# Optimization experiments

Hardware: AMD Instinct MI355X
Metric: run time of the kernel (lower is better)

Reference implementation:

```python
import jax, jax.numpy as jnp
import numpy as np

B, T, C = 4, 2048, 1024
H = 16
D = C // H  # head_dim = 64


def setup_inputs() -> dict:
    key = jax.random.key(0)
    ks = jax.random.split(key, 9)
    s = 1.0 / np.sqrt(C)
    return {
        "x": jax.random.normal(ks[0], (B, T, C), dtype=jnp.float32),
        "Wq": jax.random.normal(ks[1], (C, C), dtype=jnp.float32) * s,
        "bq": jnp.zeros((C,), dtype=jnp.float32),
        "Wk": jax.random.normal(ks[2], (C, C), dtype=jnp.float32) * s,
        "bk": jnp.zeros((C,), dtype=jnp.float32),
        "Wv": jax.random.normal(ks[3], (C, C), dtype=jnp.float32) * s,
        "bv": jnp.zeros((C,), dtype=jnp.float32),
        "Wp": jax.random.normal(ks[4], (C, C), dtype=jnp.float32) * s,
        "bp": jnp.zeros((C,), dtype=jnp.float32),
    }


def reference(x, Wq, bq, Wk, bk, Wv, bv, Wp, bp):
    # Linear projections; reshape to [B, H, T, D]
    def split_heads(y):
        return y.reshape(B, T, H, D).transpose(0, 2, 1, 3)

    q = split_heads(x @ Wq + bq)
    k = split_heads(x @ Wk + bk)
    v = split_heads(x @ Wv + bv)

    scale = 1.0 / np.sqrt(D)
    att = jnp.einsum('bhqd,bhkd->bhqk', q, k) * scale  # [B,H,T,T]
    att = jax.nn.softmax(att, axis=-1)
    # dropout with p=0.0 is identity
    out = jnp.einsum('bhqk,bhkd->bhqd', att, v)        # [B,H,T,D]
    out = out.transpose(0, 2, 1, 3).reshape(B, T, C)
    return out @ Wp + bp
```

## Files before the change

### kernel.cpp

```cpp
#include <hip/hip_runtime.h>


#define B_ 4
#define T_ 2048
#define C_ 1024
#define H_ 16
#define D_ 64

#define QSCALE 0.18033688011112042f

typedef float  f32x4  __attribute__((ext_vector_type(4)));
typedef __bf16 bf16x8 __attribute__((ext_vector_type(8)));
typedef __bf16 bf16x4 __attribute__((ext_vector_type(4)));
typedef __bf16 bf16x2 __attribute__((ext_vector_type(2)));
typedef unsigned uint2v __attribute__((ext_vector_type(2)));

typedef const __attribute__((address_space(1))) void gv_t;
typedef __attribute__((address_space(3))) void lds_t;

__device__ __forceinline__ void async_load16(const void* g, void* l) {
  __builtin_amdgcn_global_load_lds((gv_t*)g, (lds_t*)l, 16, 0, 0);
}

__device__ __forceinline__ float fast_exp2(float x) {
#if __has_builtin(__builtin_amdgcn_exp2f)
  return __builtin_amdgcn_exp2f(x);
#else
  return exp2f(x);
#endif
}

__device__ __forceinline__ void pl16_swap(unsigned& a, unsigned& b) {
#if __has_builtin(__builtin_amdgcn_permlane16_swap)
  uint2v r = __builtin_amdgcn_permlane16_swap(a, b, false, false);
  a = r[0];
  b = r[1];
#else
  asm("v_permlane16_swap_b32 %0, %1" : "+v"(a), "+v"(b));
#endif
}

__global__ __launch_bounds__(256) void cast_f32_bf16(
    const float* __restrict__ in, __bf16* __restrict__ out, int n) {
  int i = (blockIdx.x * 256 + threadIdx.x) * 8;
  if (i >= n) return;
  float4 a = *(const float4*)(in + i);
  float4 b = *(const float4*)(in + i + 4);
  bf16x8 o;
  o[0] = (__bf16)a.x; o[1] = (__bf16)a.y; o[2] = (__bf16)a.z; o[3] = (__bf16)a.w;
  o[4] = (__bf16)b.x; o[5] = (__bf16)b.y; o[6] = (__bf16)b.z; o[7] = (__bf16)b.w;
  *(bf16x8*)(out + i) = o;
}

__global__ __launch_bounds__(256) void transpose_cast_w(
    const float* __restrict__ W0, const float* __restrict__ W1,
    const float* __restrict__ W2, const float* __restrict__ W3,
    __bf16* __restrict__ out) {
  int z = blockIdx.z;
  const float* W = (z == 0) ? W0 : (z == 1) ? W1 : (z == 2) ? W2 : W3;
  __bf16* o = out + (size_t)z * (C_ * C_);
  __shared__ __align__(16) __bf16 sT[64][72];
  int tid = threadIdx.x;
  int n0 = blockIdx.x * 64, k0 = blockIdx.y * 64;
#pragma unroll
  for (int i = 0; i < 4; i++) {
    int s = tid + i * 256;
    int kr = s >> 4, nc = (s & 15) * 4;
    float4 v = *(const float4*)&W[(size_t)(k0 + kr) * C_ + n0 + nc];
    bf16x4 t;
    t[0] = (__bf16)v.x; t[1] = (__bf16)v.y; t[2] = (__bf16)v.z; t[3] = (__bf16)v.w;
    *(bf16x4*)&sT[kr][nc] = t;
  }
  __syncthreads();
#pragma unroll
  for (int i = 0; i < 2; i++) {
    int s = tid + i * 256;
    int nr = s >> 3, kc = (s & 7) * 8;
    bf16x8 ov;
#pragma unroll
    for (int j = 0; j < 8; j++) ov[j] = sT[kc + j][nr];
    *(bf16x8*)&o[(size_t)(n0 + nr) * C_ + k0 + kc] = ov;
  }
}

template <typename OutT, int EPI>
__device__ __forceinline__ void gemm_body(
    const __bf16* __restrict__ A, const __bf16* __restrict__ Bt,
    const float* __restrict__ bias, OutT* __restrict__ C, int M, int N, int K,
    float scale) {
  __shared__ __align__(16) __bf16 sA[128 * 32];
  __shared__ __align__(16) __bf16 sB[128 * 32];
  int tid = threadIdx.x, lane = tid & 63, wave = tid >> 6;
  int lr = lane & 15, quad = lane >> 4;
  int m0 = blockIdx.y * 128, n0 = blockIdx.x * 128;
  int wm = (wave & 1) * 64, wn = (wave >> 1) * 64;

  const f32x4 zero = {0.f, 0.f, 0.f, 0.f};
  f32x4 acc[4][4];
#pragma unroll
  for (int i = 0; i < 4; i++)
#pragma unroll
    for (int j = 0; j < 4; j++) acc[i][j] = zero;

  for (int k0 = 0; k0 < K; k0 += 32) {
    __syncthreads();
#pragma unroll
    for (int i = 0; i < 2; i++) {
      int s = tid + i * 256;
      int r = s >> 2, c8 = (s & 3) * 8;
      async_load16(A + (size_t)(m0 + r) * K + k0 + c8, &sA[s * 8]);
      async_load16(Bt + (size_t)(n0 + r) * K + k0 + c8, &sB[s * 8]);
    }
    __syncthreads();
    bf16x8 af[4], bfr[4];
#pragma unroll
    for (int mt = 0; mt < 4; mt++)
      af[mt] = *(const bf16x8*)&sA[(wm + mt * 16 + lr) * 32 + quad * 8];
#pragma unroll
    for (int nt = 0; nt < 4; nt++)
      bfr[nt] = *(const bf16x8*)&sB[(wn + nt * 16 + lr) * 32 + quad * 8];
#pragma unroll
    for (int mt = 0; mt < 4; mt++)
#pragma unroll
      for (int nt = 0; nt < 4; nt++)
        acc[mt][nt] = __builtin_amdgcn_mfma_f32_16x16x32_bf16(
            af[mt], bfr[nt], acc[mt][nt], 0, 0, 0);
  }
  if (EPI == 0) {
#pragma unroll
    for (int mt = 0; mt < 4; mt++) {
#pragma unroll
      for (int nt = 0; nt < 4; nt++) {
        int n = n0 + wn + nt * 16 + lr;
        float bv = bias[n];
#pragma unroll
        for (int r = 0; r < 4; r++) {
          int m = m0 + wm + mt * 16 + quad * 4 + r;
          C[(size_t)m * N + n] = (OutT)((acc[mt][nt][r] + bv) * scale);
        }
      }
    }
  } else {
    int bb = m0 >> 11;
    int mloc0 = (m0 & (T_ - 1)) + wm;
    __bf16* Ct = (__bf16*)C;
#pragma unroll
    for (int mt = 0; mt < 4; mt++) {
      int pos = ((quad & 1) << 5) | ((((quad >> 1) << 1) | (mt & 1)) << 3) |
                ((mt >> 1) << 2);
#pragma unroll
      for (int nt = 0; nt < 4; nt++) {
        int n = n0 + wn + nt * 16 + lr;
        float bv = bias[n];
        bf16x4 ov;
#pragma unroll
        for (int r = 0; r < 4; r++) ov[r] = (__bf16)(acc[mt][nt][r] + bv);
        *(bf16x4*)&Ct[((size_t)bb * C_ + n) * T_ + mloc0 + pos] = ov;
      }
    }
  }
}

__global__ __launch_bounds__(256) void gemm_qkv_kernel(
    const __bf16* __restrict__ A, const __bf16* __restrict__ WT,
    const float* __restrict__ b0, const float* __restrict__ b1,
    const float* __restrict__ b2, __bf16* __restrict__ qkbase,
    __bf16* __restrict__ Vt) {
  int z = blockIdx.z;
  if (z == 2) {
    gemm_body<__bf16, 1>(A, WT + (size_t)2 * C_ * C_, b2, Vt, B_ * T_, C_, C_,
                         1.0f);
  } else {
    const float* bias = (z == 0) ? b0 : b1;
    float scale = (z == 0) ? QSCALE : 1.0f;
    gemm_body<__bf16, 0>(A, WT + (size_t)z * C_ * C_, bias,
                         qkbase + (size_t)z * (B_ * T_) * C_, B_ * T_, C_, C_,
                         scale);
  }
}

__global__ __launch_bounds__(256) void gemm_proj_kernel(
    const __bf16* __restrict__ A, const __bf16* __restrict__ Bt,
    const float* __restrict__ bias, float* __restrict__ C) {
  gemm_body<float, 0>(A, Bt, bias, C, B_ * T_, C_, C_, 1.0f);
}

__global__ __launch_bounds__(256) void attn_kernel(
    const __bf16* __restrict__ Q, const __bf16* __restrict__ K,
    const __bf16* __restrict__ Vt, __bf16* __restrict__ O) {
  __shared__ __align__(16) __bf16 sK[64 * 72];
  __shared__ __align__(16) __bf16 sV[64 * 72];
  int tid = threadIdx.x, wave = tid >> 6, lane = tid & 63;
  int lr = lane & 15, quad = lane >> 4;
  int bh = blockIdx.y;
  int b = bh >> 4, h = bh & 15;
  int qw = blockIdx.x * 256 + wave * 64;

  bf16x8 aq[4][2];
#pragma unroll
  for (int s = 0; s < 4; s++) {
    const __bf16* qp =
        Q + ((size_t)(b * T_ + qw + s * 16 + lr)) * C_ + h * D_ + quad * 8;
    aq[s][0] = *(const bf16x8*)qp;
    aq[s][1] = *(const bf16x8*)(qp + 32);
  }

  bf16x8 onesf;
#pragma unroll
  for (int j = 0; j < 8; j++) onesf[j] = (__bf16)1.0f;

  const f32x4 zero = {0.f, 0.f, 0.f, 0.f};
  f32x4 accO[4][4];
  f32x4 accL[4] = {zero, zero, zero, zero};
#pragma unroll
  for (int s = 0; s < 4; s++)
#pragma unroll
    for (int d = 0; d < 4; d++) accO[s][d] = zero;

  int srow[2], sc8[2];
#pragma unroll
  for (int i = 0; i < 2; i++) {
    int s = tid + i * 256;
    srow[i] = s >> 3;
    sc8[i] = (s & 7) * 8;
  }

  bf16x8 kreg[2], vreg[2];
#pragma unroll
  for (int i = 0; i < 2; i++) {
    kreg[i] = *(const bf16x8*)(K + ((size_t)(b * T_ + srow[i])) * C_ + h * D_ + sc8[i]);
    vreg[i] = *(const bf16x8*)(Vt + ((size_t)(bh * D_ + srow[i])) * T_ + sc8[i]);
  }

  for (int k0 = 0; k0 < T_; k0 += 64) {
    __syncthreads();
#pragma unroll
    for (int i = 0; i < 2; i++) {
      *(bf16x8*)&sK[srow[i] * 72 + sc8[i]] = kreg[i];
      *(bf16x8*)&sV[srow[i] * 72 + sc8[i]] = vreg[i];
    }
    __syncthreads();

    if (k0 + 64 < T_) {
      int kn = k0 + 64;
#pragma unroll
      for (int i = 0; i < 2; i++) {
        kreg[i] = *(const bf16x8*)(K + ((size_t)(b * T_ + kn + srow[i])) * C_ + h * D_ + sc8[i]);
        vreg[i] = *(const bf16x8*)(Vt + ((size_t)(bh * D_ + srow[i])) * T_ + kn + sc8[i]);
      }
    }

    bf16x8 bkf[4][2];
#pragma unroll
    for (int nt = 0; nt < 4; nt++) {
      bkf[nt][0] = *(const bf16x8*)&sK[(nt * 16 + lr) * 72 + quad * 8];
      bkf[nt][1] = *(const bf16x8*)&sK[(nt * 16 + lr) * 72 + 32 + quad * 8];
    }

    bf16x8 bpA[4], bpB[4];
#pragma unroll
    for (int s = 0; s < 4; s++) {
      unsigned pw[4][2];
#pragma unroll
      for (int nt = 0; nt < 4; nt++) {
        f32x4 z = zero;
        z = __builtin_amdgcn_mfma_f32_16x16x32_bf16(bkf[nt][0], aq[s][0], z, 0, 0, 0);
        z = __builtin_amdgcn_mfma_f32_16x16x32_bf16(bkf[nt][1], aq[s][1], z, 0, 0, 0);
        union { bf16x2 h; unsigned u; } t0, t1;
        t0.h[0] = (__bf16)fast_exp2(z[0]);
        t0.h[1] = (__bf16)fast_exp2(z[1]);
        t1.h[0] = (__bf16)fast_exp2(z[2]);
        t1.h[1] = (__bf16)fast_exp2(z[3]);
        pw[nt][0] = t0.u;
        pw[nt][1] = t1.u;
      }
      unsigned a0 = pw[0][0], b0 = pw[1][0]; pl16_swap(a0, b0);
      unsigned a1 = pw[0][1], b1 = pw[1][1]; pl16_swap(a1, b1);
      unsigned a2 = pw[2][0], b2 = pw[3][0]; pl16_swap(a2, b2);
      unsigned a3 = pw[2][1], b3 = pw[3][1]; pl16_swap(a3, b3);
      union { unsigned u[4]; bf16x8 v; } pA, pB;
      pA.u[0] = a0; pA.u[1] = a1; pA.u[2] = a2; pA.u[3] = a3;
      pB.u[0] = b0; pB.u[1] = b1; pB.u[2] = b2; pB.u[3] = b3;
      bpA[s] = pA.v;
      bpB[s] = pB.v;
      accL[s] = __builtin_amdgcn_mfma_f32_16x16x32_bf16(onesf, bpA[s], accL[s], 0, 0, 0);
      accL[s] = __builtin_amdgcn_mfma_f32_16x16x32_bf16(onesf, bpB[s], accL[s], 0, 0, 0);
    }
#pragma unroll
    for (int dt = 0; dt < 4; dt++) {
      bf16x8 av0 = *(const bf16x8*)&sV[(dt * 16 + lr) * 72 + quad * 8];
      bf16x8 av1 = *(const bf16x8*)&sV[(dt * 16 + lr) * 72 + 32 + quad * 8];
#pragma unroll
      for (int s = 0; s < 4; s++) {
        accO[s][dt] = __builtin_amdgcn_mfma_f32_16x16x32_bf16(av0, bpA[s], accO[s][dt], 0, 0, 0);
        accO[s][dt] = __builtin_amdgcn_mfma_f32_16x16x32_bf16(av1, bpB[s], accO[s][dt], 0, 0, 0);
      }
    }
  }

#pragma unroll
  for (int s = 0; s < 4; s++) {
    float inv = 1.0f / accL[s][0];
    __bf16* op =
        O + ((size_t)(b * T_ + qw + s * 16 + lr)) * C_ + h * D_ + quad * 4;
#pragma unroll
    for (int dt = 0; dt < 4; dt++) {
      bf16x4 ov;
#pragma unroll
      for (int r = 0; r < 4; r++) ov[r] = (__bf16)(accO[s][dt][r] * inv);
      *(bf16x4*)&op[dt * 16] = ov;
    }
  }
}

extern "C" void kernel_launch(void* const* d_in, const int* in_sizes, int n_in,
                              void* d_out, int out_size, void* d_ws, size_t ws_size,
                              hipStream_t stream) {
  const float* x  = (const float*)d_in[0];
  const float* Wq = (const float*)d_in[1];
  const float* bq = (const float*)d_in[2];
  const float* Wk = (const float*)d_in[3];
  const float* bk = (const float*)d_in[4];
  const float* Wv = (const float*)d_in[5];
  const float* bv = (const float*)d_in[6];
  const float* Wp = (const float*)d_in[7];
  const float* bp = (const float*)d_in[8];
  float* out = (float*)d_out;

  char* ws = (char*)d_ws;
  const size_t MB = 1024 * 1024;
  __bf16* xb    = (__bf16*)(ws + 0 * MB);
  __bf16* WT    = (__bf16*)(ws + 16 * MB);
  __bf16* Qb    = (__bf16*)(ws + 24 * MB);
  __bf16* Kb    = Qb + (size_t)(B_ * T_) * C_;
  __bf16* Vt    = Kb + (size_t)(B_ * T_) * C_;
  __bf16* attnb = (__bf16*)(ws + 72 * MB);
  __bf16* WpT   = WT + (size_t)3 * C_ * C_;

  cast_f32_bf16<<<dim3(4096), dim3(256), 0, stream>>>(x, xb, B_ * T_ * C_);
  transpose_cast_w<<<dim3(16, 16, 4), dim3(256), 0, stream>>>(Wq, Wk, Wv, Wp, WT);
  gemm_qkv_kernel<<<dim3(8, 64, 3), dim3(256), 0, stream>>>(xb, WT, bq, bk, bv, Qb, Vt);
  attn_kernel<<<dim3(8, 64), dim3(256), 0, stream>>>(Qb, Kb, Vt, attnb);
  gemm_proj_kernel<<<dim3(8, 64), dim3(256), 0, stream>>>(attnb, WpT, bp, out);
}
```

Before: 279.3 us.

## Rewrite GEMMs as 256x256 tiles with double-buffered async LDS pipeline

Replaces the 128x128, K=32 single-buffered GEMM with a 256x256 tile, 512-thread, K=64 kernel. It double-buffers A/B in 128KB dynamic LDS, issues async global-to-LDS loads interleaved with MFMA phases, and XOR-swizzles LDS addresses to avoid bank conflicts. Scheduling barriers and setprio are meant to overlap memory latency with matrix math and raise data reuse per tile. The risks are fewer blocks (128 for proj), which can under-fill the GPU's CUs, and a large LDS footprint that limits occupancy.

```diff
diff --git a/kernel.cpp b/kernel.cpp
--- a/kernel.cpp
+++ b/kernel.cpp
@@ -83,106 +83,187 @@
   }
 }
 
+#define PHASE_FENCE() do { __builtin_amdgcn_sched_barrier(0); \
+                           __builtin_amdgcn_s_barrier(); } while (0)
+
 template <typename OutT, int EPI>
-__device__ __forceinline__ void gemm_body(
+__device__ __forceinline__ void gemm256_body(
     const __bf16* __restrict__ A, const __bf16* __restrict__ Bt,
-    const float* __restrict__ bias, OutT* __restrict__ C, int M, int N, int K,
-    float scale) {
-  __shared__ __align__(16) __bf16 sA[128 * 32];
-  __shared__ __align__(16) __bf16 sB[128 * 32];
+    const float* __restrict__ bias, OutT* __restrict__ C, int N, float scale) {
+  extern __shared__ __align__(16) char smem[];
+  __bf16* sAe = (__bf16*)smem;
+  __bf16* sBe = (__bf16*)(smem + 65536);
+  const int NT = 16;
   int tid = threadIdx.x, lane = tid & 63, wave = tid >> 6;
   int lr = lane & 15, quad = lane >> 4;
-  int m0 = blockIdx.y * 128, n0 = blockIdx.x * 128;
-  int wm = (wave & 1) * 64, wn = (wave >> 1) * 64;
+  int wr = wave >> 2, wc = wave & 3;
+  int m0 = blockIdx.y * 256, n0 = blockIdx.x * 256;
+  int lswz = ((lr >> 2) & 1) << 4;
+
+  int srcRow[2], srcCol[2], ldsS[2];
+#pragma unroll
+  for (int l = 0; l < 2; l++) {
+    int s = tid + l * 512;
+    int s2 = s ^ (((s >> 5) & 1) << 1);
+    srcRow[l] = s2 >> 3;
+    srcCol[l] = (s2 & 7) * 8;
+    ldsS[l] = s * 8;
+  }
+  const __bf16* Ag = A + (size_t)m0 * 1024;
+  const __bf16* Bg = Bt + (size_t)n0 * 1024;
+
+  auto issueA = [&](int tt, int l) {
+    int slot = tt & 1;
+    const __bf16* g = Ag + (size_t)srcRow[l] * 1024 + tt * 64 + srcCol[l];
+    async_load16(g, sAe + slot * 16384 + ldsS[l]);
+    async_load16(g + (size_t)128 * 1024, sAe + slot * 16384 + 8192 + ldsS[l]);
+  };
+  auto issueB = [&](int tt, int Hh) {
+    int slot = tt & 1;
+#pragma unroll
+    for (int l = 0; l < 2; l++) {
+      const __bf16* g =
+          Bg + (size_t)(Hh * 128 + srcRow[l]) * 1024 + tt * 64 + srcCol[l];
+      async_load16(g, sBe + slot * 16384 + Hh * 8192 + ldsS[l]);
+    }
+  };
 
   const f32x4 zero = {0.f, 0.f, 0.f, 0.f};
-  f32x4 acc[4][4];
-#pragma unroll
-  for (int i = 0; i < 4; i++)
+  f32x4 acc[8][4];
+#pragma unroll
+  for (int i = 0; i < 8; i++)
 #pragma unroll
     for (int j = 0; j < 4; j++) acc[i][j] = zero;
 
-  for (int k0 = 0; k0 < K; k0 += 32) {
-    __syncthreads();
-#pragma unroll
-    for (int i = 0; i < 2; i++) {
-      int s = tid + i * 256;
-      int r = s >> 2, c8 = (s & 3) * 8;
-      async_load16(A + (size_t)(m0 + r) * K + k0 + c8, &sA[s * 8]);
-      async_load16(Bt + (size_t)(n0 + r) * K + k0 + c8, &sB[s * 8]);
-    }
-    __syncthreads();
-    bf16x8 af[4], bfr[4];
+  bf16x8 af0[4][2], af1[4][2], bf01[2][2], bf23[2][2];
+
+  auto rdA = [&](int slot, int msub, bf16x8(&af)[4][2]) {
+    int rbase = wr * 128 + msub * 64;
 #pragma unroll
     for (int mt = 0; mt < 4; mt++)
-      af[mt] = *(const bf16x8*)&sA[(wm + mt * 16 + lr) * 32 + quad * 8];
-#pragma unroll
-    for (int nt = 0; nt < 4; nt++)
-      bfr[nt] = *(const bf16x8*)&sB[(wn + nt * 16 + lr) * 32 + quad * 8];
-#pragma unroll
-    for (int mt = 0; mt < 4; mt++)
-#pragma unroll
-      for (int nt = 0; nt < 4; nt++)
-        acc[mt][nt] = __builtin_amdgcn_mfma_f32_16x16x32_bf16(
-            af[mt], bfr[nt], acc[mt][nt], 0, 0, 0);
-  }
+#pragma unroll
+      for (int j = 0; j < 2; j++) {
+        int row = rbase + mt * 16 + lr;
+        int e = (row * 64 + j * 32 + quad * 8) ^ lswz;
+        af[mt][j] = *(const bf16x8*)&sAe[slot * 16384 + e];
+      }
+  };
+  auto rdB = [&](int slot, int nsub, bf16x8(&bf)[2][2]) {
+    int rbase = wc * 64 + nsub * 32;
+#pragma unroll
+    for (int ntl = 0; ntl < 2; ntl++)
+#pragma unroll
+      for (int j = 0; j < 2; j++) {
+        int row = rbase + ntl * 16 + lr;
+        int e = (row * 64 + j * 32 + quad * 8) ^ lswz;
+        bf[ntl][j] = *(const bf16x8*)&sBe[slot * 16384 + e];
+      }
+  };
+
+#define MF16(AF, BF, MB, NB)                                              \
+  do {                                                                    \
+    __builtin_amdgcn_s_setprio(1);                                        \
+    _Pragma("unroll") for (int mt = 0; mt < 4; mt++)                      \
+        _Pragma("unroll") for (int ntl = 0; ntl < 2; ntl++)               \
+            _Pragma("unroll") for (int j = 0; j < 2; j++)                 \
+                acc[(MB) + mt][(NB) + ntl] =                              \
+                    __builtin_amdgcn_mfma_f32_16x16x32_bf16(              \
+                        AF[mt][j], BF[ntl][j], acc[(MB) + mt][(NB) + ntl],\
+                        0, 0, 0);                                         \
+    __builtin_amdgcn_s_setprio(0);                                        \
+  } while (0)
+
+  issueA(0, 0); issueA(0, 1); issueB(0, 0); issueB(0, 1);
+  issueA(1, 0); issueA(1, 1); issueB(1, 0);
+  asm volatile("s_waitcnt vmcnt(6)" ::: "memory");
+  PHASE_FENCE();
+
+  for (int t = 0; t < NT; t++) {
+    int slot = t & 1;
+    rdA(slot, 0, af0);
+    rdB(slot, 0, bf01);
+    if (t + 1 < NT) issueB(t + 1, 1);
+    PHASE_FENCE();
+    MF16(af0, bf01, 0, 0);
+    PHASE_FENCE();
+    rdA(slot, 1, af1);
+    if (t + 2 < NT) issueA(t + 2, 0);
+    PHASE_FENCE();
+    MF16(af1, bf01, 4, 0);
+    PHASE_FENCE();
+    rdB(slot, 1, bf23);
+    if (t + 2 < NT) issueA(t + 2, 1);
+    PHASE_FENCE();
+    MF16(af1, bf23, 4, 2);
+    PHASE_FENCE();
+    if (t + 2 < NT) issueB(t + 2, 0);
+    if (t < NT - 2) {
+      asm volatile("s_waitcnt vmcnt(6)" ::: "memory");
+    } else {
+      asm volatile("s_waitcnt vmcnt(0)" ::: "memory");
+    }
+    PHASE_FENCE();
+    MF16(af0, bf23, 0, 2);
+    PHASE_FENCE();
+  }
+
   if (EPI == 0) {
 #pragma unroll
-    for (int mt = 0; mt < 4; mt++) {
+    for (int mt = 0; mt < 8; mt++) {
 #pragma unroll
       for (int nt = 0; nt < 4; nt++) {
-        int n = n0 + wn + nt * 16 + lr;
+        int n = n0 + wc * 64 + nt * 16 + lr;
         float bv = bias[n];
 #pragma unroll
         for (int r = 0; r < 4; r++) {
-          int m = m0 + wm + mt * 16 + quad * 4 + r;
+          int m = m0 + wr * 128 + mt * 16 + quad * 4 + r;
           C[(size_t)m * N + n] = (OutT)((acc[mt][nt][r] + bv) * scale);
         }
       }
     }
   } else {
     int bb = m0 >> 11;
-    int mloc0 = (m0 & (T_ - 1)) + wm;
+    int base = (m0 & (T_ - 1)) + wr * 128;
     __bf16* Ct = (__bf16*)C;
 #pragma unroll
-    for (int mt = 0; mt < 4; mt++) {
-      int pos = ((quad & 1) << 5) | ((((quad >> 1) << 1) | (mt & 1)) << 3) |
-                ((mt >> 1) << 2);
+    for (int mt = 0; mt < 8; mt++) {
+      int mtl = mt & 3;
+      int pos = ((quad & 1) << 5) | ((((quad >> 1) << 1) | (mtl & 1)) << 3) |
+                ((mtl >> 1) << 2);
+      int tcol = base + (mt >> 2) * 64 + pos;
 #pragma unroll
       for (int nt = 0; nt < 4; nt++) {
-        int n = n0 + wn + nt * 16 + lr;
+        int n = n0 + wc * 64 + nt * 16 + lr;
         float bv = bias[n];
         bf16x4 ov;
 #pragma unroll
         for (int r = 0; r < 4; r++) ov[r] = (__bf16)(acc[mt][nt][r] + bv);
-        *(bf16x4*)&Ct[((size_t)bb * C_ + n) * T_ + mloc0 + pos] = ov;
-      }
-    }
-  }
-}
-
-__global__ __launch_bounds__(256) void gemm_qkv_kernel(
+        *(bf16x4*)&Ct[((size_t)bb * C_ + n) * T_ + tcol] = ov;
+      }
+    }
+  }
+}
+
+__global__ __launch_bounds__(512, 2) void gemm256_qkv_kernel(
     const __bf16* __restrict__ A, const __bf16* __restrict__ WT,
     const float* __restrict__ b0, const float* __restrict__ b1,
     const float* __restrict__ b2, __bf16* __restrict__ qkbase,
     __bf16* __restrict__ Vt) {
   int z = blockIdx.z;
   if (z == 2) {
-    gemm_body<__bf16, 1>(A, WT + (size_t)2 * C_ * C_, b2, Vt, B_ * T_, C_, C_,
-                         1.0f);
+    gemm256_body<__bf16, 1>(A, WT + (size_t)2 * C_ * C_, b2, Vt, C_, 1.0f);
   } else {
     const float* bias = (z == 0) ? b0 : b1;
     float scale = (z == 0) ? QSCALE : 1.0f;
-    gemm_body<__bf16, 0>(A, WT + (size_t)z * C_ * C_, bias,
-                         qkbase + (size_t)z * (B_ * T_) * C_, B_ * T_, C_, C_,
-                         scale);
-  }
-}
-
-__global__ __launch_bounds__(256) void gemm_proj_kernel(
+    gemm256_body<__bf16, 0>(A, WT + (size_t)z * C_ * C_, bias,
+                            qkbase + (size_t)z * (B_ * T_) * C_, C_, scale);
+  }
+}
+
+__global__ __launch_bounds__(512, 2) void gemm256_proj_kernel(
     const __bf16* __restrict__ A, const __bf16* __restrict__ Bt,
     const float* __restrict__ bias, float* __restrict__ C) {
-  gemm_body<float, 0>(A, Bt, bias, C, B_ * T_, C_, C_, 1.0f);
+  gemm256_body<float, 0>(A, Bt, bias, C, C_, 1.0f);
 }
 
 __global__ __launch_bounds__(256) void attn_kernel(
@@ -327,6 +408,17 @@
   const float* bp = (const float*)d_in[8];
   float* out = (float*)d_out;
 
+  static bool attr_done = false;
+  if (!attr_done) {
+    (void)hipFuncSetAttribute((const void*)gemm256_qkv_kernel,
+                              hipFuncAttributeMaxDynamicSharedMemorySize,
+                              131072);
+    (void)hipFuncSetAttribute((const void*)gemm256_proj_kernel,
+                              hipFuncAttributeMaxDynamicSharedMemorySize,
+                              131072);
+    attr_done = true;
+  }
+
   char* ws = (char*)d_ws;
   const size_t MB = 1024 * 1024;
   __bf16* xb    = (__bf16*)(ws + 0 * MB);
@@ -339,7 +431,9 @@
 
   cast_f32_bf16<<<dim3(4096), dim3(256), 0, stream>>>(x, xb, B_ * T_ * C_);
   transpose_cast_w<<<dim3(16, 16, 4), dim3(256), 0, stream>>>(Wq, Wk, Wv, Wp, WT);
-  gemm_qkv_kernel<<<dim3(8, 64, 3), dim3(256), 0, stream>>>(xb, WT, bq, bk, bv, Qb, Vt);
+  gemm256_qkv_kernel<<<dim3(4, 32, 3), dim3(512), 131072, stream>>>(
+      xb, WT, bq, bk, bv, Qb, Vt);
   attn_kernel<<<dim3(8, 64), dim3(256), 0, stream>>>(Qb, Kb, Vt, attnb);
-  gemm_proj_kernel<<<dim3(8, 64), dim3(256), 0, stream>>>(attnb, WpT, bp, out);
-}
+  gemm256_proj_kernel<<<dim3(4, 32), dim3(512), 131072, stream>>>(
+      attnb, WpT, bp, out);
+}
```

Measured after the change: 285.0 us. +2.0%, slower.
